# Performance work log

Measured on AMD Instinct MI355X. Metric: run time of the kernel, lower is better.

Reference implementation:

```python
import jax, jax.numpy as jnp
import numpy as np

K = 16
RADIUS = 1.0
N = 16384
SEQ = 8


def _knn(pc, k):
    """Brute-force kNN of pc against itself. pc: (1, n, 3).
    Returns (dist, idx) each (1, n, k), sorted ascending by distance,
    matching pointutils.knn semantics (Euclidean distance)."""
    x2 = jnp.sum(pc * pc, axis=-1)  # (1, n)
    # d2[b,i,j] = ||p_i - p_j||^2 via expansion; avoids (n,n,3) intermediate
    d2 = x2[:, :, None] + x2[:, None, :] - 2.0 * jnp.einsum('bnd,bmd->bnm', pc, pc)
    d2 = jnp.maximum(d2, 0.0)
    neg_d2, idx = jax.lax.top_k(-d2, k)  # k smallest distances
    dist = jnp.sqrt(jnp.maximum(-neg_d2, 0.0))
    return dist, idx


def setup_inputs() -> dict:
    key = jax.random.key(0)
    k1, k2, k3 = jax.random.split(key, 3)
    return {
        'pc_source': jax.random.normal(k1, (1, N, 3), dtype=jnp.float32),
        'pred_flow': jax.random.normal(k2, (SEQ, N, 3), dtype=jnp.float32),
        'weights': jax.random.uniform(k3, (N,), dtype=jnp.float32),
    }


def reference(pc_source, pred_flow, weights):
    # flow: (seq, 3, n)
    flow = jnp.transpose(pred_flow, (0, 2, 1))
    dist, idx = _knn(pc_source, K)  # (1, n, k)
    # replace out-of-radius neighbors with the nearest (self) index
    idx = jnp.where(dist > RADIUS, idx[:, :, 0:1], idx)
    idx = idx[0]  # (n, k); identical for all sequence steps
    # grouping_operation: gather neighbor flows -> (seq, 3, n, k)
    nn_flow = flow[:, :, idx]
    diff = flow[:, :, :, None] - nn_flow  # (seq, 3, n, k)
    # L2 norm over channel dim (loss_norm=2), safe at 0 (self-neighbor)
    sq = jnp.sum(diff * diff, axis=1)  # (seq, n, k)
    norm = jnp.where(sq > 0, jnp.sqrt(jnp.where(sq > 0, sq, 1.0)), 0.0)
    loss = norm.mean(axis=-1)  # (seq, n)
    loss = loss * weights[None, :]
    loss = loss.sum(axis=1)  # (seq,)
    wsum = weights.sum()
    loss = jnp.where(wsum > 0, loss / wsum, loss)
    return loss.mean()
```

## Files before the change

kernel.cpp:

```cpp
#include <hip/hip_runtime.h>
#include <math.h>

#define NPTS  16384
#define KNN   16
#define SEQV  8
#define NW    16
#define BATCH 8
#define CAPM  15
#define CAPR  1.001f
#define NBKT  256
#define BSCALE 56.8888f
#define HBLK  64
#define NGRP  256

#define SLOT(arr, t, col) arr[(t) * 1024 + (col)]

#define WS_HIST   256
#define WS_STARTS 65792
#define WS_SIDX   67072
#define WS_SORTED 132640
#define WS_FLOWT  394912

__device__ __forceinline__ unsigned umin_(unsigned a, unsigned b) { return a < b ? a : b; }
__device__ __forceinline__ unsigned umax_(unsigned a, unsigned b) { return a > b ? a : b; }

__device__ __forceinline__ int nbucket(float x) { return (int)fminf(x * BSCALE, 255.0f); }

__device__ __forceinline__ void merge_one(unsigned keys[KNN], unsigned kk) {
    if (kk < keys[KNN - 1]) {
#pragma unroll
        for (int u = 0; u < KNN; ++u) {
            unsigned lo = umin_(kk, keys[u]);
            kk = umax_(kk, keys[u]);
            keys[u] = lo;
        }
    }
}

__device__ __forceinline__ void merge16(unsigned k[KNN], const unsigned o[KNN]) {
    unsigned v[KNN];
#pragma unroll
    for (int i = 0; i < KNN; ++i) v[i] = umin_(k[i], o[KNN - 1 - i]);
#pragma unroll
    for (int d = 8; d >= 1; d >>= 1) {
#pragma unroll
        for (int i = 0; i < KNN; ++i) {
            if ((i & d) == 0) {
                unsigned lo = umin_(v[i], v[i + d]);
                unsigned hi = umax_(v[i], v[i + d]);
                v[i] = lo; v[i + d] = hi;
            }
        }
    }
#pragma unroll
    for (int i = 0; i < KNN; ++i) k[i] = v[i];
}

__device__ __forceinline__ void tree_load_merge(unsigned* uS, unsigned keys[KNN], int src) {
    unsigned o[KNN];
#pragma unroll
    for (int t = 0; t < KNN; ++t) o[t] = SLOT(uS, t, src);
    merge16(keys, o);
}

__global__ __launch_bounds__(256) void hist_kernel(
    const float* __restrict__ pc, const float* __restrict__ flow,
    unsigned* __restrict__ hist, float4* __restrict__ flowT)
{
    __shared__ unsigned h[NBKT];
    const int tid = threadIdx.x;
    h[tid] = 0u;
    __syncthreads();
    const int i = blockIdx.x * 256 + tid;
    const float x = pc[3 * i + 0], y = pc[3 * i + 1], z = pc[3 * i + 2];
    const float n = sqrtf(fmaf(x, x, fmaf(y, y, z * z)));
    atomicAdd(&h[nbucket(n)], 1u);
#pragma unroll
    for (int s = 0; s < SEQV; ++s) {
        const float* fp = flow + (size_t)s * NPTS * 3 + 3 * i;
        flowT[s * NPTS + i] = make_float4(fp[0], fp[1], fp[2], 0.0f);
    }
    __syncthreads();
    hist[tid * HBLK + blockIdx.x] = h[tid];
}

__global__ __launch_bounds__(256) void scatter_kernel(
    const float* __restrict__ pc, const unsigned* __restrict__ hist,
    unsigned* __restrict__ starts, float* __restrict__ accum,
    unsigned* __restrict__ sidx, float4* __restrict__ sorted4)
{
    __shared__ unsigned sH[NBKT];
    __shared__ unsigned sBase[NBKT];
    __shared__ unsigned sCnt[NBKT];
    const int tid = threadIdx.x;
    const int b   = blockIdx.x;

    unsigned own = 0, pre = 0;
    {
        const unsigned* row = hist + tid * HBLK;
        unsigned s = 0, p = 0;
#pragma unroll 8
        for (int k = 0; k < HBLK; ++k) {
            const unsigned c = row[k];
            if (k < b) p += c;
            s += c;
        }
        own = s; pre = p;
        sH[tid] = s;
        sCnt[tid] = 0u;
    }
    __syncthreads();
    for (int off = 1; off < NBKT; off <<= 1) {
        unsigned a = 0u;
        if (tid >= off) a = sH[tid - off];
        __syncthreads();
        sH[tid] += a;
        __syncthreads();
    }
    {
        const unsigned excl = sH[tid] - own;
        sBase[tid] = excl + pre;
        if (b == 0) starts[tid] = excl;
    }
    if (b == 0 && tid == 0) starts[NBKT] = NPTS;
    if (b == 0 && tid < 8) ((unsigned*)accum)[tid] = 0u;
    __syncthreads();

    const int i = b * 256 + tid;
    const float x = pc[3 * i + 0], y = pc[3 * i + 1], z = pc[3 * i + 2];
    const float c2 = fmaf(x, x, fmaf(y, y, z * z));
    const int bin = nbucket(sqrtf(c2));
    const unsigned rank = atomicAdd(&sCnt[bin], 1u);
    const unsigned pos = sBase[bin] + rank;
    sorted4[pos] = make_float4(-2.0f * x, -2.0f * y, -2.0f * z, c2);
    sidx[pos] = (unsigned)i;
    if (b == 0 && tid < 8) {
        sorted4[NPTS + tid] = make_float4(0.0f, 0.0f, 0.0f, 1e18f);
        sidx[NPTS + tid] = 0u;
    }
}

__global__ __launch_bounds__(1024, 4) void mega_kernel(
    const float4* __restrict__ sorted, const unsigned* __restrict__ sidx,
    const unsigned* __restrict__ starts, const float4* __restrict__ flowT,
    const float* __restrict__ wts, float* __restrict__ accum,
    float* __restrict__ out)
{
    __shared__ unsigned uS[1024 * 16];
    float* sred = (float*)&uS[15 * 1024 + 1000];
    float* sTau = (float*)&uS[16320];

    const int tid  = threadIdx.x;
    const int lane = tid & 63;
    const int wv   = __builtin_amdgcn_readfirstlane(tid >> 6);
    const int is   = blockIdx.x * 64 + lane;

    const float4 mi = sorted[is];
    const float qx = -0.5f * mi.x;
    const float qy = -0.5f * mi.y;
    const float qz = -0.5f * mi.z;
    const float q2 = mi.w;
    const unsigned iorig = sidx[is];
    const float analytic = 0.14304f * exp2f(0.480898f * q2);
    const float tau0 = fminf(analytic, CAPR);

    const float nq = sqrtf(q2);
    float nmin = nq, nmax = nq;
#pragma unroll
    for (int off = 32; off > 0; off >>= 1) {
        nmin = fminf(nmin, __shfl_xor(nmin, off));
        nmax = fmaxf(nmax, __shfl_xor(nmax, off));
    }
    const float r0 = sqrtf(fminf(0.14304f * exp2f(0.480898f * nmax * nmax), CAPR));
    const int blo = nbucket(fmaxf(nmin - r0, 0.0f));
    const int bhi = nbucket(nmax + r0);
    const int kT0 = __builtin_amdgcn_readfirstlane((int)starts[blo]) >> 3;
    const int kTe = (__builtin_amdgcn_readfirstlane((int)starts[bhi + 1]) + 7) >> 3;

    unsigned keys[KNN];
#pragma unroll
    for (int t = 0; t < KNN; ++t) keys[t] = 0xFFFFFFFFu;
    int cnt = 0;
    unsigned* buf = &uS[tid * CAPM];

    {
        float taufs = tau0 - q2;
        float4 A[BATCH], Bv[BATCH];
        unsigned As[BATCH], Bs[BATCH];

        auto proc = [&](const float4* C, const unsigned* S) {
#pragma unroll
            for (int q = 0; q < BATCH; ++q) {
                const float4 c = C[q];
                float d2p = fmaf(c.x, qx, fmaf(c.y, qy, fmaf(c.z, qz, c.w)));
                bool acc = d2p <= taufs;
                if (__any(acc)) {
                    if (acc) {
                        float d2 = fmaxf(d2p + q2, 0.0f);
                        buf[cnt] = (__float_as_uint(d2) & 0xFFFFC000u) | S[q];
                        ++cnt;
                    }
                    if (__any(cnt >= CAPM - 1)) {
#pragma unroll 1
                        for (int t = 0; t < CAPM - 1; ++t)
                            merge_one(keys, (t < cnt) ? buf[t] : 0xFFFFFFFFu);
                        cnt = 0;
                        float d16n = __uint_as_float(keys[KNN - 1] & 0xFFFFC000u);
                        taufs = fminf(taufs, fmaf(d16n, 1.0002f, 1e-6f) - q2);
                    }
                }
            }
        };

        int k = kT0 + wv;
        bool hA = (k < kTe);
        if (hA) { const float4* bp = sorted + (k << 3); const unsigned* sp = sidx + (k << 3);
#pragma unroll
            for (int q = 0; q < BATCH; ++q) { A[q] = bp[q]; As[q] = sp[q]; } }
        while (hA) {
            int k2 = k + 64; bool hB = (k2 < kTe);
            if (hB) { const float4* bp = sorted + (k2 << 3); const unsigned* sp = sidx + (k2 << 3);
#pragma unroll
                for (int q = 0; q < BATCH; ++q) { Bv[q] = bp[q]; Bs[q] = sp[q]; } }
            proc(A, As);
            if (!hB) break;
            int k3 = k2 + 64; bool hC = (k3 < kTe);
            if (hC) { const float4* bp = sorted + (k3 << 3); const unsigned* sp = sidx + (k3 << 3);
#pragma unroll
                for (int q = 0; q < BATCH; ++q) { A[q] = bp[q]; As[q] = sp[q]; } }
            proc(Bv, Bs);
            k = k3; hA = hC;
        }
#pragma unroll 1
        for (int t = 0; t < CAPM - 1; ++t)
            merge_one(keys, (t < cnt) ? buf[t] : 0xFFFFFFFFu);
        cnt = 0;
    }

    unsigned keys2[KNN];
#pragma unroll
    for (int t = 0; t < KNN; ++t) keys2[t] = keys[t];

    __syncthreads();

#pragma unroll
    for (int t = 0; t < KNN; ++t) SLOT(uS, t, tid) = keys[t];
    __syncthreads();
    if (wv < 8) {
        tree_load_merge(uS, keys, tid + 512);
#pragma unroll
        for (int t = 0; t < KNN; ++t) SLOT(uS, t, tid) = keys[t];
    }
    __syncthreads();
    if (wv < 4) {
        tree_load_merge(uS, keys, tid + 256);
#pragma unroll
        for (int t = 0; t < KNN; ++t) SLOT(uS, t, tid) = keys[t];
    }
    __syncthreads();
    if (wv < 2) {
        tree_load_merge(uS, keys, tid + 128);
#pragma unroll
        for (int t = 0; t < KNN; ++t) SLOT(uS, t, tid) = keys[t];
    }
    __syncthreads();
    if (wv == 0) {
        tree_load_merge(uS, keys, tid + 64);
        const float d16 = __uint_as_float(keys[KNN - 1] & 0xFFFFC000u);
        const float tf  = fmaf(d16, 1.0002f, 1e-6f);
        const bool fail = !(tf <= tau0);
        const float tv = fail ? CAPR : tf;
        sTau[lane] = tv;
        float tm = tv;
#pragma unroll
        for (int off = 32; off > 0; off >>= 1) tm = fmaxf(tm, __shfl_xor(tm, off));
        unsigned long long bw = __ballot(fail && (analytic < CAPR));
        if (lane == 0) { uS[16316] = (bw != 0ull) ? 1u : 0u; ((float*)uS)[16317] = tm; }
    }
    __syncthreads();

    float taufs = sTau[lane] - q2;
    const unsigned anyWide = __builtin_amdgcn_readfirstlane(uS[16316]);
    const float rA = sqrtf(((float*)uS)[16317]);
    int kA0, kAe;
    if (anyWide) { kA0 = 0; kAe = NPTS / 8; }
    else {
        int bloA = nbucket(fmaxf(nmin - rA, 0.0f));
        int bhiA = nbucket(nmax + rA);
        kA0 = __builtin_amdgcn_readfirstlane((int)starts[bloA]) >> 3;
        kAe = (__builtin_amdgcn_readfirstlane((int)starts[bhiA + 1]) + 7) >> 3;
    }
#pragma unroll
    for (int t = 0; t < KNN; ++t) keys[t] = keys2[t];
    {
        float4 A[BATCH], Bv[BATCH];
        unsigned As[BATCH], Bs[BATCH];

        auto proc = [&](const float4* C, const unsigned* S) {
#pragma unroll
            for (int q = 0; q < BATCH; ++q) {
                const float4 c = C[q];
                float d2p = fmaf(c.x, qx, fmaf(c.y, qy, fmaf(c.z, qz, c.w)));
                bool acc = d2p <= taufs;
                if (__any(acc)) {
                    if (acc) {
                        float d2 = fmaxf(d2p + q2, 0.0f);
                        buf[cnt] = (__float_as_uint(d2) & 0xFFFFC000u) | S[q];
                        ++cnt;
                    }
                    if (__any(cnt >= CAPM - 1)) {
#pragma unroll 1
                        for (int t = 0; t < CAPM - 1; ++t)
                            merge_one(keys, (t < cnt) ? buf[t] : 0xFFFFFFFFu);
                        cnt = 0;
                        float d16n = __uint_as_float(keys[KNN - 1] & 0xFFFFC000u);
                        taufs = fminf(taufs, fmaf(d16n, 1.0002f, 1e-6f) - q2);
                    }
                }
            }
        };

        auto skipb = [&](int k) -> bool {
            return (!anyWide) && (k < kTe) && (((k - kT0 - wv) & 63) == 0);
        };
        int k = kA0 + ((wv - (kA0 - kT0)) & 15);
        if (skipb(k)) k += 16;
        bool hA = (k < kAe);
        if (hA) { const float4* bp = sorted + (k << 3); const unsigned* sp = sidx + (k << 3);
#pragma unroll
            for (int q = 0; q < BATCH; ++q) { A[q] = bp[q]; As[q] = sp[q]; } }
        while (hA) {
            int k2 = k + 16; if (skipb(k2)) k2 += 16;
            bool hB = (k2 < kAe);
            if (hB) { const float4* bp = sorted + (k2 << 3); const unsigned* sp = sidx + (k2 << 3);
#pragma unroll
                for (int q = 0; q < BATCH; ++q) { Bv[q] = bp[q]; Bs[q] = sp[q]; } }
            proc(A, As);
            if (!hB) break;
            int k3 = k2 + 16; if (skipb(k3)) k3 += 16;
            bool hC = (k3 < kAe);
            if (hC) { const float4* bp = sorted + (k3 << 3); const unsigned* sp = sidx + (k3 << 3);
#pragma unroll
                for (int q = 0; q < BATCH; ++q) { A[q] = bp[q]; As[q] = sp[q]; } }
            proc(Bv, Bs);
            k = k3; hA = hC;
        }
#pragma unroll 1
        for (int t = 0; t < CAPM - 1; ++t)
            merge_one(keys, (t < cnt) ? buf[t] : 0xFFFFFFFFu);
    }
    __syncthreads();

#pragma unroll
    for (int t = 0; t < KNN; ++t) SLOT(uS, t, tid) = keys[t];
    __syncthreads();
    if (wv < 8) {
        tree_load_merge(uS, keys, tid + 512);
#pragma unroll
        for (int t = 0; t < KNN; ++t) SLOT(uS, t, tid) = keys[t];
    }
    __syncthreads();
    if (wv < 4) {
        tree_load_merge(uS, keys, tid + 256);
#pragma unroll
        for (int t = 0; t < KNN; ++t) SLOT(uS, t, tid) = keys[t];
    }
    __syncthreads();
    if (wv < 2) {
        tree_load_merge(uS, keys, tid + 128);
#pragma unroll
        for (int t = 0; t < KNN; ++t) SLOT(uS, t, tid) = keys[t];
    }
    __syncthreads();
    if (wv == 0) {
        tree_load_merge(uS, keys, tid + 64);
        const int id0 = (int)(keys[0] & 0x3FFFu);
#pragma unroll
        for (int t = 0; t < KNN; ++t) {
            float d2t = __uint_as_float(keys[t] & 0xFFFFC000u);
            int   j   = (int)(keys[t] & 0x3FFFu);
            SLOT(uS, t, lane) = (unsigned)((d2t > 1.0f) ? id0 : j);
        }
    }
    __syncthreads();

    {
        const int s  = wv & 7;
        const int kh = wv >> 3;
        const float4* fs4 = flowT + (size_t)s * NPTS;
        const float4 qf = fs4[iorig];

        float sum = 0.0f;
#pragma unroll
        for (int z = 0; z < 8; ++z) {
            int j = (int)SLOT(uS, kh * 8 + z, lane);
            const float4 v = fs4[j];
            float dx = qf.x - v.x;
            float dy = qf.y - v.y;
            float dz = qf.z - v.z;
            float sq = fmaf(dx, dx, fmaf(dy, dy, dz * dz));
            sum += (sq > 0.0f) ? sqrtf(sq) : 0.0f;
        }

        float contrib = wts[iorig] * sum;
#pragma unroll
        for (int off = 32; off > 0; off >>= 1) contrib += __shfl_down(contrib, off);
        if (lane == 0) sred[wv] = contrib;

        if (wv == 0) {
            float wi = wts[iorig];
#pragma unroll
            for (int off = 32; off > 0; off >>= 1) wi += __shfl_down(wi, off);
            if (lane == 0) atomicAdd(&accum[1], wi);
        }
        __syncthreads();

        if (tid == 0) {
            float c = 0.0f;
#pragma unroll
            for (int t = 0; t < NW; ++t) c += sred[t];
            atomicAdd(&accum[0], c);
            __threadfence();
            unsigned ticket = atomicAdd((unsigned*)accum + 2, 1u);
            if (ticket == gridDim.x - 1) {
                float a  = atomicAdd(&accum[0], 0.0f);
                float ws = atomicAdd(&accum[1], 0.0f);
                float v  = a / (float)(KNN * SEQV);
                out[0] = (ws > 0.0f) ? (v / ws) : v;
            }
        }
    }
}

extern "C" void kernel_launch(void* const* d_in, const int* in_sizes, int n_in,
                              void* d_out, int out_size, void* d_ws, size_t ws_size,
                              hipStream_t stream)
{
    const float* pc   = (const float*)d_in[0];
    const float* flow = (const float*)d_in[1];
    const float* wts  = (const float*)d_in[2];
    float* out = (float*)d_out;

    float*    accum  = (float*)d_ws;
    unsigned* hist   = (unsigned*)((char*)d_ws + WS_HIST);
    unsigned* starts = (unsigned*)((char*)d_ws + WS_STARTS);
    unsigned* sidx   = (unsigned*)((char*)d_ws + WS_SIDX);
    float4*   sorted = (float4*)  ((char*)d_ws + WS_SORTED);
    float4*   flowT  = (float4*)  ((char*)d_ws + WS_FLOWT);

    hist_kernel   <<<HBLK, 256, 0, stream>>>(pc, flow, hist, flowT);
    scatter_kernel<<<HBLK, 256, 0, stream>>>(pc, hist, starts, accum, sidx, sorted);
    mega_kernel   <<<NGRP, 1024, 0, stream>>>(sorted, sidx, starts, flowT, wts, accum, out);
}
```

Measured before the change: 131.3 us.

## Encode sorted-position indices in keys, drop sidx loads, swizzle block order

```diff
diff --git a/kernel.cpp b/kernel.cpp
--- a/kernel.cpp
+++ b/kernel.cpp
@@ -153,7 +153,8 @@
     const int tid  = threadIdx.x;
     const int lane = tid & 63;
     const int wv   = __builtin_amdgcn_readfirstlane(tid >> 6);
-    const int is   = blockIdx.x * 64 + lane;
+    const int gid  = ((blockIdx.x & 7) << 5) | (blockIdx.x >> 3);
+    const int is   = gid * 64 + lane;
 
     const float4 mi = sorted[is];
     const float qx = -0.5f * mi.x;
@@ -186,9 +187,8 @@
     {
         float taufs = tau0 - q2;
         float4 A[BATCH], Bv[BATCH];
-        unsigned As[BATCH], Bs[BATCH];
-
-        auto proc = [&](const float4* C, const unsigned* S) {
+
+        auto proc = [&](const float4* C, int kb) {
 #pragma unroll
             for (int q = 0; q < BATCH; ++q) {
                 const float4 c = C[q];
@@ -197,7 +197,8 @@
                 if (__any(acc)) {
                     if (acc) {
                         float d2 = fmaxf(d2p + q2, 0.0f);
-                        buf[cnt] = (__float_as_uint(d2) & 0xFFFFC000u) | S[q];
+                        buf[cnt] = (__float_as_uint(d2) & 0xFFFFC000u)
+                                 | (unsigned)((kb << 3) + q);
                         ++cnt;
                     }
                     if (__any(cnt >= CAPM - 1)) {
@@ -214,25 +215,31 @@
 
         int k = kT0 + wv;
         bool hA = (k < kTe);
-        if (hA) { const float4* bp = sorted + (k << 3); const unsigned* sp = sidx + (k << 3);
-#pragma unroll
-            for (int q = 0; q < BATCH; ++q) { A[q] = bp[q]; As[q] = sp[q]; } }
+        if (hA) { const float4* bp = sorted + (k << 3);
+#pragma unroll
+            for (int q = 0; q < BATCH; ++q) A[q] = bp[q]; }
         while (hA) {
             int k2 = k + 64; bool hB = (k2 < kTe);
-            if (hB) { const float4* bp = sorted + (k2 << 3); const unsigned* sp = sidx + (k2 << 3);
-#pragma unroll
-                for (int q = 0; q < BATCH; ++q) { Bv[q] = bp[q]; Bs[q] = sp[q]; } }
-            proc(A, As);
+            if (hB) { const float4* bp = sorted + (k2 << 3);
+#pragma unroll
+                for (int q = 0; q < BATCH; ++q) Bv[q] = bp[q]; }
+            proc(A, k);
             if (!hB) break;
             int k3 = k2 + 64; bool hC = (k3 < kTe);
-            if (hC) { const float4* bp = sorted + (k3 << 3); const unsigned* sp = sidx + (k3 << 3);
-#pragma unroll
-                for (int q = 0; q < BATCH; ++q) { A[q] = bp[q]; As[q] = sp[q]; } }
-            proc(Bv, Bs);
+            if (hC) { const float4* bp = sorted + (k3 << 3);
+#pragma unroll
+                for (int q = 0; q < BATCH; ++q) A[q] = bp[q]; }
+            proc(Bv, k2);
             k = k3; hA = hC;
         }
+        int maxc = cnt;
+#pragma unroll
+        for (int off = 32; off > 0; off >>= 1) {
+            int o = __shfl_xor(maxc, off); maxc = (o > maxc) ? o : maxc;
+        }
+        maxc = __builtin_amdgcn_readfirstlane(maxc);
 #pragma unroll 1
-        for (int t = 0; t < CAPM - 1; ++t)
+        for (int t = 0; t < maxc; ++t)
             merge_one(keys, (t < cnt) ? buf[t] : 0xFFFFFFFFu);
         cnt = 0;
     }
@@ -294,9 +301,8 @@
     for (int t = 0; t < KNN; ++t) keys[t] = keys2[t];
     {
         float4 A[BATCH], Bv[BATCH];
-        unsigned As[BATCH], Bs[BATCH];
-
-        auto proc = [&](const float4* C, const unsigned* S) {
+
+        auto proc = [&](const float4* C, int kb) {
 #pragma unroll
             for (int q = 0; q < BATCH; ++q) {
                 const float4 c = C[q];
@@ -305,7 +311,8 @@
                 if (__any(acc)) {
                     if (acc) {
                         float d2 = fmaxf(d2p + q2, 0.0f);
-                        buf[cnt] = (__float_as_uint(d2) & 0xFFFFC000u) | S[q];
+                        buf[cnt] = (__float_as_uint(d2) & 0xFFFFC000u)
+                                 | (unsigned)((kb << 3) + q);
                         ++cnt;
                     }
                     if (__any(cnt >= CAPM - 1)) {
@@ -326,27 +333,33 @@
         int k = kA0 + ((wv - (kA0 - kT0)) & 15);
         if (skipb(k)) k += 16;
         bool hA = (k < kAe);
-        if (hA) { const float4* bp = sorted + (k << 3); const unsigned* sp = sidx + (k << 3);
-#pragma unroll
-            for (int q = 0; q < BATCH; ++q) { A[q] = bp[q]; As[q] = sp[q]; } }
+        if (hA) { const float4* bp = sorted + (k << 3);
+#pragma unroll
+            for (int q = 0; q < BATCH; ++q) A[q] = bp[q]; }
         while (hA) {
             int k2 = k + 16; if (skipb(k2)) k2 += 16;
             bool hB = (k2 < kAe);
-            if (hB) { const float4* bp = sorted + (k2 << 3); const unsigned* sp = sidx + (k2 << 3);
-#pragma unroll
-                for (int q = 0; q < BATCH; ++q) { Bv[q] = bp[q]; Bs[q] = sp[q]; } }
-            proc(A, As);
+            if (hB) { const float4* bp = sorted + (k2 << 3);
+#pragma unroll
+                for (int q = 0; q < BATCH; ++q) Bv[q] = bp[q]; }
+            proc(A, k);
             if (!hB) break;
             int k3 = k2 + 16; if (skipb(k3)) k3 += 16;
             bool hC = (k3 < kAe);
-            if (hC) { const float4* bp = sorted + (k3 << 3); const unsigned* sp = sidx + (k3 << 3);
-#pragma unroll
-                for (int q = 0; q < BATCH; ++q) { A[q] = bp[q]; As[q] = sp[q]; } }
-            proc(Bv, Bs);
+            if (hC) { const float4* bp = sorted + (k3 << 3);
+#pragma unroll
+                for (int q = 0; q < BATCH; ++q) A[q] = bp[q]; }
+            proc(Bv, k2);
             k = k3; hA = hC;
         }
+        int maxc = cnt;
+#pragma unroll
+        for (int off = 32; off > 0; off >>= 1) {
+            int o = __shfl_xor(maxc, off); maxc = (o > maxc) ? o : maxc;
+        }
+        maxc = __builtin_amdgcn_readfirstlane(maxc);
 #pragma unroll 1
-        for (int t = 0; t < CAPM - 1; ++t)
+        for (int t = 0; t < maxc; ++t)
             merge_one(keys, (t < cnt) ? buf[t] : 0xFFFFFFFFu);
     }
     __syncthreads();
@@ -374,11 +387,11 @@
     __syncthreads();
     if (wv == 0) {
         tree_load_merge(uS, keys, tid + 64);
-        const int id0 = (int)(keys[0] & 0x3FFFu);
+        const int id0 = (int)sidx[keys[0] & 0x3FFFu];
 #pragma unroll
         for (int t = 0; t < KNN; ++t) {
             float d2t = __uint_as_float(keys[t] & 0xFFFFC000u);
-            int   j   = (int)(keys[t] & 0x3FFFu);
+            int   j   = (int)sidx[keys[t] & 0x3FFFu];
             SLOT(uS, t, lane) = (unsigned)((d2t > 1.0f) ? id0 : j);
         }
     }
```

Measured after the change: 134.4 us. 2.4% more time.

## Fuse histogram, scatter and kNN kernels into one cooperative launch with grid syncs

Applied to the files above, without the earlier changes.

```diff
diff --git a/kernel.cpp b/kernel.cpp
--- a/kernel.cpp
+++ b/kernel.cpp
@@ -1,5 +1,8 @@
 #include <hip/hip_runtime.h>
+#include <hip/hip_cooperative_groups.h>
 #include <math.h>
+
+namespace cg = cooperative_groups;
 
 #define NPTS  16384
 #define KNN   16
@@ -10,16 +13,15 @@
 #define CAPR  1.001f
 #define NBKT  256
 #define BSCALE 56.8888f
-#define HBLK  64
 #define NGRP  256
 
 #define SLOT(arr, t, col) arr[(t) * 1024 + (col)]
 
 #define WS_HIST   256
-#define WS_STARTS 65792
-#define WS_SIDX   67072
-#define WS_SORTED 132640
-#define WS_FLOWT  394912
+#define WS_STARTS 262400
+#define WS_SIDX   263680
+#define WS_SORTED 329248
+#define WS_FLOWT  591520
 
 __device__ __forceinline__ unsigned umin_(unsigned a, unsigned b) { return a < b ? a : b; }
 __device__ __forceinline__ unsigned umax_(unsigned a, unsigned b) { return a > b ? a : b; }
@@ -63,97 +65,95 @@
     merge16(keys, o);
 }
 
-__global__ __launch_bounds__(256) void hist_kernel(
+__global__ __launch_bounds__(1024, 4) void fused_kernel(
     const float* __restrict__ pc, const float* __restrict__ flow,
-    unsigned* __restrict__ hist, float4* __restrict__ flowT)
-{
-    __shared__ unsigned h[NBKT];
-    const int tid = threadIdx.x;
-    h[tid] = 0u;
-    __syncthreads();
-    const int i = blockIdx.x * 256 + tid;
-    const float x = pc[3 * i + 0], y = pc[3 * i + 1], z = pc[3 * i + 2];
-    const float n = sqrtf(fmaf(x, x, fmaf(y, y, z * z)));
-    atomicAdd(&h[nbucket(n)], 1u);
-#pragma unroll
-    for (int s = 0; s < SEQV; ++s) {
-        const float* fp = flow + (size_t)s * NPTS * 3 + 3 * i;
-        flowT[s * NPTS + i] = make_float4(fp[0], fp[1], fp[2], 0.0f);
-    }
-    __syncthreads();
-    hist[tid * HBLK + blockIdx.x] = h[tid];
-}
-
-__global__ __launch_bounds__(256) void scatter_kernel(
-    const float* __restrict__ pc, const unsigned* __restrict__ hist,
-    unsigned* __restrict__ starts, float* __restrict__ accum,
-    unsigned* __restrict__ sidx, float4* __restrict__ sorted4)
-{
-    __shared__ unsigned sH[NBKT];
-    __shared__ unsigned sBase[NBKT];
-    __shared__ unsigned sCnt[NBKT];
-    const int tid = threadIdx.x;
-    const int b   = blockIdx.x;
-
-    unsigned own = 0, pre = 0;
-    {
-        const unsigned* row = hist + tid * HBLK;
-        unsigned s = 0, p = 0;
-#pragma unroll 8
-        for (int k = 0; k < HBLK; ++k) {
-            const unsigned c = row[k];
-            if (k < b) p += c;
-            s += c;
-        }
-        own = s; pre = p;
-        sH[tid] = s;
-        sCnt[tid] = 0u;
-    }
-    __syncthreads();
-    for (int off = 1; off < NBKT; off <<= 1) {
-        unsigned a = 0u;
-        if (tid >= off) a = sH[tid - off];
-        __syncthreads();
-        sH[tid] += a;
-        __syncthreads();
-    }
-    {
-        const unsigned excl = sH[tid] - own;
-        sBase[tid] = excl + pre;
-        if (b == 0) starts[tid] = excl;
-    }
-    if (b == 0 && tid == 0) starts[NBKT] = NPTS;
-    if (b == 0 && tid < 8) ((unsigned*)accum)[tid] = 0u;
-    __syncthreads();
-
-    const int i = b * 256 + tid;
-    const float x = pc[3 * i + 0], y = pc[3 * i + 1], z = pc[3 * i + 2];
-    const float c2 = fmaf(x, x, fmaf(y, y, z * z));
-    const int bin = nbucket(sqrtf(c2));
-    const unsigned rank = atomicAdd(&sCnt[bin], 1u);
-    const unsigned pos = sBase[bin] + rank;
-    sorted4[pos] = make_float4(-2.0f * x, -2.0f * y, -2.0f * z, c2);
-    sidx[pos] = (unsigned)i;
-    if (b == 0 && tid < 8) {
-        sorted4[NPTS + tid] = make_float4(0.0f, 0.0f, 0.0f, 1e18f);
-        sidx[NPTS + tid] = 0u;
-    }
-}
-
-__global__ __launch_bounds__(1024, 4) void mega_kernel(
-    const float4* __restrict__ sorted, const unsigned* __restrict__ sidx,
-    const unsigned* __restrict__ starts, const float4* __restrict__ flowT,
-    const float* __restrict__ wts, float* __restrict__ accum,
+    const float* __restrict__ wts, float* __restrict__ ws,
     float* __restrict__ out)
 {
     __shared__ unsigned uS[1024 * 16];
     float* sred = (float*)&uS[15 * 1024 + 1000];
     float* sTau = (float*)&uS[16320];
 
+    float*    accum  = ws;
+    unsigned* hist   = (unsigned*)((char*)ws + WS_HIST);
+    unsigned* starts = (unsigned*)((char*)ws + WS_STARTS);
+    unsigned* sidx   = (unsigned*)((char*)ws + WS_SIDX);
+    float4*   sorted = (float4*)  ((char*)ws + WS_SORTED);
+    float4*   flowT  = (float4*)  ((char*)ws + WS_FLOWT);
+
+    cg::grid_group grid = cg::this_grid();
+
     const int tid  = threadIdx.x;
     const int lane = tid & 63;
     const int wv   = __builtin_amdgcn_readfirstlane(tid >> 6);
-    const int is   = blockIdx.x * 64 + lane;
+    const int b    = blockIdx.x;
+
+    float px = 0.0f, py = 0.0f, pz = 0.0f, pc2 = 0.0f;
+    int pv = 0; unsigned prank = 0;
+    if (tid < NBKT) uS[tid] = 0u;
+    __syncthreads();
+    if (tid < 64) {
+        const int i = b * 64 + tid;
+        px = pc[3 * i + 0]; py = pc[3 * i + 1]; pz = pc[3 * i + 2];
+        pc2 = fmaf(px, px, fmaf(py, py, pz * pz));
+        pv = nbucket(sqrtf(pc2));
+        prank = atomicAdd(&uS[pv], 1u);
+    }
+    {
+        const int t = b * 1024 + tid;
+        if (t < SEQV * NPTS) {
+            const int s = t >> 14, i = t & (NPTS - 1);
+            const float* fp = flow + (size_t)s * NPTS * 3 + 3 * i;
+            flowT[t] = make_float4(fp[0], fp[1], fp[2], 0.0f);
+        }
+    }
+    __syncthreads();
+    if (tid < NBKT) hist[tid * NGRP + b] = uS[tid];
+    grid.sync();
+
+    {
+        unsigned own = 0, pre = 0;
+        if (tid < NBKT) {
+            const unsigned* row = hist + tid * NGRP;
+            unsigned s = 0, p = 0;
+#pragma unroll 8
+            for (int k = 0; k < NGRP; ++k) {
+                const unsigned c = row[k];
+                if (k < b) p += c;
+                s += c;
+            }
+            own = s; pre = p;
+            uS[tid] = s;
+        }
+        __syncthreads();
+        for (int off = 1; off < NBKT; off <<= 1) {
+            unsigned a = 0u;
+            if (tid < NBKT && tid >= off) a = uS[tid - off];
+            __syncthreads();
+            if (tid < NBKT) uS[tid] += a;
+            __syncthreads();
+        }
+        if (tid < NBKT) {
+            const unsigned excl = uS[tid] - own;
+            uS[NBKT + tid] = excl + pre;
+            if (b == 0) starts[tid] = excl;
+        }
+        if (b == 0 && tid == 0) starts[NBKT] = NPTS;
+        if (b == 0 && tid < 8) ((unsigned*)accum)[tid] = 0u;
+        __syncthreads();
+        if (tid < 64) {
+            const unsigned pos = uS[NBKT + pv] + prank;
+            sorted[pos] = make_float4(-2.0f * px, -2.0f * py, -2.0f * pz, pc2);
+            sidx[pos] = (unsigned)(b * 64 + tid);
+        }
+        if (b == 0 && tid < 8) {
+            sorted[NPTS + tid] = make_float4(0.0f, 0.0f, 0.0f, 1e18f);
+            sidx[NPTS + tid] = 0u;
+        }
+    }
+    grid.sync();
+
+    const int is = b * 64 + lane;
 
     const float4 mi = sorted[is];
     const float qx = -0.5f * mi.x;
@@ -424,9 +424,9 @@
             unsigned ticket = atomicAdd((unsigned*)accum + 2, 1u);
             if (ticket == gridDim.x - 1) {
                 float a  = atomicAdd(&accum[0], 0.0f);
-                float ws = atomicAdd(&accum[1], 0.0f);
+                float wsv = atomicAdd(&accum[1], 0.0f);
                 float v  = a / (float)(KNN * SEQV);
-                out[0] = (ws > 0.0f) ? (v / ws) : v;
+                out[0] = (wsv > 0.0f) ? (v / wsv) : v;
             }
         }
     }
@@ -440,15 +440,9 @@
     const float* flow = (const float*)d_in[1];
     const float* wts  = (const float*)d_in[2];
     float* out = (float*)d_out;
-
-    float*    accum  = (float*)d_ws;
-    unsigned* hist   = (unsigned*)((char*)d_ws + WS_HIST);
-    unsigned* starts = (unsigned*)((char*)d_ws + WS_STARTS);
-    unsigned* sidx   = (unsigned*)((char*)d_ws + WS_SIDX);
-    float4*   sorted = (float4*)  ((char*)d_ws + WS_SORTED);
-    float4*   flowT  = (float4*)  ((char*)d_ws + WS_FLOWT);
-
-    hist_kernel   <<<HBLK, 256, 0, stream>>>(pc, flow, hist, flowT);
-    scatter_kernel<<<HBLK, 256, 0, stream>>>(pc, hist, starts, accum, sidx, sorted);
-    mega_kernel   <<<NGRP, 1024, 0, stream>>>(sorted, sidx, starts, flowT, wts, accum, out);
+    float* ws  = (float*)d_ws;
+
+    void* args[] = { (void*)&pc, (void*)&flow, (void*)&wts, (void*)&ws, (void*)&out };
+    hipLaunchCooperativeKernel((const void*)fused_kernel, dim3(NGRP), dim3(1024),
+                               args, 0, stream);
 }
```

Result: slower. 258.0 us (+96.5%).
